# Performance work log

Hardware: AMD Instinct MI355X
Metric: run time of the kernel (lower is better)

The kernel has to match this reference:

```python
import jax, jax.numpy as jnp
import numpy as np

# module hyperparameters (from init_kwargs)
K = 32          # out_channels / features per branch
THRESH = 20.0   # firing threshold
KWTA = 4        # winners per branch
RF = 512        # rf_size (number of branches)
L = 2048        # receptive-field length
T = 32          # timesteps (leading 'batch' dim in SpykeTorch)
C = 1           # in_channels


def setup_inputs() -> dict:
    key = jax.random.key(0)
    k1, k2, k3 = jax.random.split(key, 3)
    rec_field = jax.random.uniform(k1, (T, C, RF, L), dtype=jnp.float32)
    W = jax.random.normal(k2, (RF, K, C, L), dtype=jnp.float32)  # per-branch local-conv weights
    reward = jax.random.normal(k3, (1, 1, RF), dtype=jnp.float32)
    return {"rec_field": rec_field, "W": W, "reward": reward}


def _winner_mask(thr, spikes):
    """SpykeTorch sf.get_k_winners for a single branch with 1x1 spatial output.
    thr, spikes: (T, K) thresholded potentials and their sign (0/1).
    Returns a (K,) 0/1 mask over the kwta winning features.
    Score = earliest-spike-dominant total potential, exactly as in SpykeTorch:
      first  = T - sum_t spikes           (first spike time, clamped)
      values = thr[first, k]
      total  = sum_t (spikes*values + spikes * max(spikes*values)*T)
    With 1x1 spatial, inhibition_radius has no effect; picking then zeroing a
    feature == distinct top-k over features with a nonzero check.
    """
    first = jnp.clip((T - spikes.sum(0)).astype(jnp.int32), 0, T - 1)          # (K,)
    vals_at_first = jnp.take_along_axis(thr, first[None, :], axis=0)[0]        # (K,)
    trunc = spikes * vals_at_first[None, :]                                    # (T, K)
    v = trunc.max() * T
    total = (trunc + spikes * v).sum(0)                                        # (K,)
    top_vals, top_idx = jax.lax.top_k(total, KWTA)
    valid = (top_vals != 0).astype(thr.dtype)
    return jnp.zeros((K,), thr.dtype).at[top_idx].max(valid)


def reference(rec_field, W, reward):
    # per-branch local convolution: kernel covers the whole (1,L) input -> 1x1 output
    pot = jnp.einsum('tcrl,rkcl->rtk', rec_field, W)        # (RF, T, K)
    # sf.fire: keep potentials strictly above threshold (F.threshold semantics)
    thr = jnp.where(pot > THRESH, pot, jnp.zeros((), pot.dtype))
    spikes = jnp.sign(thr)
    # kWTA winner masks per branch (coefs), then masked sign
    mask = jax.vmap(_winner_mask)(thr, spikes)              # (RF, K)
    out = jnp.sign(thr * mask[:, None, :])                  # (RF, T, K)
    # torch: cat(dim=2) -> (T,K,RF,1) -> squeeze -> (T,K,RF) -> unsqueeze(1) -> (T,1,K,RF)
    return jnp.transpose(out, (1, 2, 0))[:, None, :, :]
```

## Files before the change

kernel.cpp:

```cpp
#include <hip/hip_runtime.h>
#include <cstdint>


#define RFN 512
#define TN  32
#define KN  32
#define LN  2048
#define CHUNK 128
#define NITER (LN / CHUNK)

__global__ __launch_bounds__(256, 2) void column1_kernel(
    const float* __restrict__ rec,
    const float* __restrict__ wgt,
    float* __restrict__ out)
{
    __shared__ __align__(16) float lds[2 * 64 * CHUNK];
    const int r    = blockIdx.x;
    const int tid  = threadIdx.x;
    const int lane = tid & 63;
    const int wv   = tid >> 6;
    const int tg   = lane >> 3;
    const int kg   = lane & 7;

    const int c4 = tid & 31;
    const int r0 = tid >> 5;
    const float* gsrc[8];
    int ldoff[8];
#pragma unroll
    for (int s = 0; s < 8; ++s) {
        const int row = r0 + 8 * s;
        const float* g;
        if (row < 32) g = rec + ((size_t)(row * RFN + r)) * LN + (c4 << 2);
        else          g = wgt + ((size_t)(r * KN + (row - 32))) * LN + (c4 << 2);
        gsrc[s]  = g;
        ldoff[s] = row * CHUNK + ((c4 ^ (row & 7)) << 2);
    }

    float4 stage[8];
#pragma unroll
    for (int s = 0; s < 8; ++s) stage[s] = *(const float4*)gsrc[s];

    float acc[4][4];
#pragma unroll
    for (int jt = 0; jt < 4; ++jt)
#pragma unroll
        for (int jk = 0; jk < 4; ++jk) acc[jt][jk] = 0.0f;

    int p = 0;
    for (int it = 0; it < NITER; ++it) {
        float* buf = lds + p * (64 * CHUNK);
#pragma unroll
        for (int s = 0; s < 8; ++s) *(float4*)(buf + ldoff[s]) = stage[s];
        __syncthreads();
        if (it + 1 < NITER) {
#pragma unroll
            for (int s = 0; s < 8; ++s) {
                gsrc[s] += CHUNK;
                stage[s] = *(const float4*)gsrc[s];
            }
        }
        const float* rs = buf;
        const float* ws = buf + 32 * CHUNK;
#pragma unroll
        for (int q = 0; q < 8; ++q) {
            const int qg = (wv << 3) + q;
            float4 a[4], b[4];
#pragma unroll
            for (int j = 0; j < 4; ++j)
                a[j] = *(const float4*)(rs + (tg + 8 * j) * CHUNK + ((qg ^ tg) << 2));
#pragma unroll
            for (int j = 0; j < 4; ++j)
                b[j] = *(const float4*)(ws + (kg + 8 * j) * CHUNK + ((qg ^ kg) << 2));
#pragma unroll
            for (int jt = 0; jt < 4; ++jt)
#pragma unroll
                for (int jk = 0; jk < 4; ++jk) {
                    float v0 = fmaf(a[jt].x, b[jk].x, acc[jt][jk]);
                    v0 = fmaf(a[jt].y, b[jk].y, v0);
                    v0 = fmaf(a[jt].z, b[jk].z, v0);
                    acc[jt][jk] = fmaf(a[jt].w, b[jk].w, v0);
                }
        }
        p ^= 1;
    }

    float* red = lds;
#pragma unroll
    for (int jt = 0; jt < 4; ++jt)
#pragma unroll
        for (int jk = 0; jk < 4; ++jk)
            red[(wv << 10) + (tg + 8 * jt) * 32 + (kg + 8 * jk)] = acc[jt][jk];
    __syncthreads();

    float* thr_s = lds + 4096;
#pragma unroll
    for (int e = 0; e < 4; ++e) {
        const int o = (tid << 2) + e;
        float pv = red[o] + red[1024 + o] + red[2048 + o] + red[3072 + o];
        float th = (pv > 20.0f) ? pv : 0.0f;
        thr_s[(o >> 5) * 33 + (o & 31)] = th;
    }
    __syncthreads();

    float* nspk_s = lds + 4096 + 1056;
    float* vals_s = nspk_s + 32;
    float* cand_s = vals_s + 32;
    float* tot_s  = cand_s + 32;
    float* mask_s = tot_s + 32;

    if (tid < 32) {
        const int k = tid;
        int ns = 0;
        for (int t = 0; t < 32; ++t) ns += (thr_s[t * 33 + k] > 0.0f) ? 1 : 0;
        int first = 32 - ns; if (first > 31) first = 31;
        const float vf = thr_s[first * 33 + k];
        nspk_s[k] = (float)ns;
        vals_s[k] = vf;
        cand_s[k] = (ns > 0) ? vf : 0.0f;
        mask_s[k] = 0.0f;
    }
    __syncthreads();

    if (tid == 0) {
        float vm = 0.0f;
        for (int k = 0; k < 32; ++k) vm = fmaxf(vm, cand_s[k]);
        const float v = vm * 32.0f;
        for (int k = 0; k < 32; ++k) tot_s[k] = nspk_s[k] * (vals_s[k] + v);
        for (int sel = 0; sel < 4; ++sel) {
            int best = 0; float bv = -1.0f;
            for (int k = 0; k < 32; ++k) {
                const float tv = tot_s[k];
                if (tv > bv) { bv = tv; best = k; }
            }
            if (bv > 0.0f) mask_s[best] = 1.0f;
            tot_s[best] = -1.0f;
        }
    }
    __syncthreads();

#pragma unroll
    for (int e = 0; e < 4; ++e) {
        const int o = (tid << 2) + e;
        const int t = o >> 5, k = o & 31;
        out[(size_t)t * (KN * RFN) + k * RFN + r] =
            (thr_s[t * 33 + k] > 0.0f && mask_s[k] > 0.0f) ? 1.0f : 0.0f;
    }
}

extern "C" void kernel_launch(void* const* d_in, const int* in_sizes, int n_in,
                              void* d_out, int out_size, void* d_ws, size_t ws_size,
                              hipStream_t stream) {
    const float* rec = (const float*)d_in[0];
    const float* wgt = (const float*)d_in[1];
    float* out = (float*)d_out;
    column1_kernel<<<dim3(RFN), dim3(256), 0, stream>>>(rec, wgt, out);
}
```

Measured before the change: 324.1 us.

## Split reduction dimension across four blocks and add separate epilogue kernel

Each branch's 2048-length dot product is split into four segments handled by separate blocks, giving 2048 blocks instead of 512. Partial 32x32 results go to a workspace buffer, and a second kernel sums them and runs the threshold and k-winner selection. The chunk size is halved and the swizzle widened, which lowers shared memory per block and allows a higher occupancy hint. The aim is to fill the GPU's compute units and hide memory latency better on this bandwidth-bound load, at the cost of a second launch and a small workspace round trip.

After: 330.0 us. Within noise of the previous version (+1.8%).

```diff
diff --git a/kernel.cpp b/kernel.cpp
--- a/kernel.cpp
+++ b/kernel.cpp
@@ -6,39 +6,44 @@
 #define TN  32
 #define KN  32
 #define LN  2048
-#define CHUNK 128
-#define NITER (LN / CHUNK)
+#define SPLIT 4
+#define LSEG (LN / SPLIT)
+#define CHUNK 64
+#define NITER (LSEG / CHUNK)
 
-__global__ __launch_bounds__(256, 2) void column1_kernel(
+__global__ __launch_bounds__(256, 5) void column1_gemm(
     const float* __restrict__ rec,
     const float* __restrict__ wgt,
-    float* __restrict__ out)
+    float* __restrict__ wsout)
 {
     __shared__ __align__(16) float lds[2 * 64 * CHUNK];
-    const int r    = blockIdx.x;
+    const int bs   = blockIdx.x;
+    const int r    = bs >> 2;
+    const int sseg = bs & 3;
+    const int l0   = sseg * LSEG;
     const int tid  = threadIdx.x;
     const int lane = tid & 63;
     const int wv   = tid >> 6;
     const int tg   = lane >> 3;
     const int kg   = lane & 7;
 
-    const int c4 = tid & 31;
-    const int r0 = tid >> 5;
-    const float* gsrc[8];
-    int ldoff[8];
+    const int c4 = tid & 15;
+    const int r0 = tid >> 4;
+    const float* gsrc[4];
+    int ldoff[4];
 #pragma unroll
-    for (int s = 0; s < 8; ++s) {
-        const int row = r0 + 8 * s;
+    for (int s = 0; s < 4; ++s) {
+        const int row = r0 + 16 * s;
         const float* g;
-        if (row < 32) g = rec + ((size_t)(row * RFN + r)) * LN + (c4 << 2);
-        else          g = wgt + ((size_t)(r * KN + (row - 32))) * LN + (c4 << 2);
+        if (row < 32) g = rec + ((size_t)(row * RFN + r)) * LN + l0 + (c4 << 2);
+        else          g = wgt + ((size_t)(r * KN + (row - 32))) * LN + l0 + (c4 << 2);
         gsrc[s]  = g;
-        ldoff[s] = row * CHUNK + ((c4 ^ (row & 7)) << 2);
+        ldoff[s] = row * CHUNK + ((c4 ^ (row & 15)) << 2);
     }
 
-    float4 stage[8];
+    float4 stage[4];
 #pragma unroll
-    for (int s = 0; s < 8; ++s) stage[s] = *(const float4*)gsrc[s];
+    for (int s = 0; s < 4; ++s) stage[s] = *(const float4*)gsrc[s];
 
     float acc[4][4];
 #pragma unroll
@@ -50,27 +55,31 @@
     for (int it = 0; it < NITER; ++it) {
         float* buf = lds + p * (64 * CHUNK);
 #pragma unroll
-        for (int s = 0; s < 8; ++s) *(float4*)(buf + ldoff[s]) = stage[s];
+        for (int s = 0; s < 4; ++s) *(float4*)(buf + ldoff[s]) = stage[s];
         __syncthreads();
         if (it + 1 < NITER) {
 #pragma unroll
-            for (int s = 0; s < 8; ++s) {
+            for (int s = 0; s < 4; ++s) {
                 gsrc[s] += CHUNK;
                 stage[s] = *(const float4*)gsrc[s];
             }
         }
         const float* rs = buf;
-        const float* ws = buf + 32 * CHUNK;
+        const float* wsh = buf + 32 * CHUNK;
 #pragma unroll
-        for (int q = 0; q < 8; ++q) {
-            const int qg = (wv << 3) + q;
+        for (int q = 0; q < 4; ++q) {
+            const int qg = (wv << 2) + q;
             float4 a[4], b[4];
 #pragma unroll
-            for (int j = 0; j < 4; ++j)
-                a[j] = *(const float4*)(rs + (tg + 8 * j) * CHUNK + ((qg ^ tg) << 2));
+            for (int j = 0; j < 4; ++j) {
+                const int row = tg + 8 * j;
+                a[j] = *(const float4*)(rs + row * CHUNK + ((qg ^ (row & 15)) << 2));
+            }
 #pragma unroll
-            for (int j = 0; j < 4; ++j)
-                b[j] = *(const float4*)(ws + (kg + 8 * j) * CHUNK + ((qg ^ kg) << 2));
+            for (int j = 0; j < 4; ++j) {
+                const int row = kg + 8 * j;
+                b[j] = *(const float4*)(wsh + row * CHUNK + ((qg ^ (row & 15)) << 2));
+            }
 #pragma unroll
             for (int jt = 0; jt < 4; ++jt)
 #pragma unroll
@@ -92,21 +101,45 @@
             red[(wv << 10) + (tg + 8 * jt) * 32 + (kg + 8 * jk)] = acc[jt][jk];
     __syncthreads();
 
-    float* thr_s = lds + 4096;
+    const int o = tid << 2;
+    float4 p0 = *(const float4*)(red + o);
+    float4 p1 = *(const float4*)(red + 1024 + o);
+    float4 p2 = *(const float4*)(red + 2048 + o);
+    float4 p3 = *(const float4*)(red + 3072 + o);
+    float4 pv;
+    pv.x = p0.x + p1.x + p2.x + p3.x;
+    pv.y = p0.y + p1.y + p2.y + p3.y;
+    pv.z = p0.z + p1.z + p2.z + p3.z;
+    pv.w = p0.w + p1.w + p2.w + p3.w;
+    *(float4*)(wsout + (size_t)(r * SPLIT + sseg) * 1024 + o) = pv;
+}
+
+__global__ __launch_bounds__(256) void column1_epilogue(
+    const float* __restrict__ wsin,
+    float* __restrict__ out)
+{
+    __shared__ float thr_s[32 * 33];
+    __shared__ float nspk_s[32], vals_s[32], cand_s[32], tot_s[32], mask_s[32];
+    const int r   = blockIdx.x;
+    const int tid = threadIdx.x;
+    const float* base = wsin + (size_t)r * (SPLIT * 1024);
+
+    const int o = tid << 2;
+    float4 p0 = *(const float4*)(base + o);
+    float4 p1 = *(const float4*)(base + 1024 + o);
+    float4 p2 = *(const float4*)(base + 2048 + o);
+    float4 p3 = *(const float4*)(base + 3072 + o);
+    float pv[4] = { p0.x + p1.x + p2.x + p3.x,
+                    p0.y + p1.y + p2.y + p3.y,
+                    p0.z + p1.z + p2.z + p3.z,
+                    p0.w + p1.w + p2.w + p3.w };
 #pragma unroll
     for (int e = 0; e < 4; ++e) {
-        const int o = (tid << 2) + e;
-        float pv = red[o] + red[1024 + o] + red[2048 + o] + red[3072 + o];
-        float th = (pv > 20.0f) ? pv : 0.0f;
-        thr_s[(o >> 5) * 33 + (o & 31)] = th;
+        const int oo = o + e;
+        const float th = (pv[e] > 20.0f) ? pv[e] : 0.0f;
+        thr_s[(oo >> 5) * 33 + (oo & 31)] = th;
     }
     __syncthreads();
-
-    float* nspk_s = lds + 4096 + 1056;
-    float* vals_s = nspk_s + 32;
-    float* cand_s = vals_s + 32;
-    float* tot_s  = cand_s + 32;
-    float* mask_s = tot_s + 32;
 
     if (tid < 32) {
         const int k = tid;
@@ -140,8 +173,8 @@
 
 #pragma unroll
     for (int e = 0; e < 4; ++e) {
-        const int o = (tid << 2) + e;
-        const int t = o >> 5, k = o & 31;
+        const int oo = o + e;
+        const int t = oo >> 5, k = oo & 31;
         out[(size_t)t * (KN * RFN) + k * RFN + r] =
             (thr_s[t * 33 + k] > 0.0f && mask_s[k] > 0.0f) ? 1.0f : 0.0f;
     }
@@ -153,5 +186,7 @@
     const float* rec = (const float*)d_in[0];
     const float* wgt = (const float*)d_in[1];
     float* out = (float*)d_out;
-    column1_kernel<<<dim3(RFN), dim3(256), 0, stream>>>(rec, wgt, out);
+    float* ws  = (float*)d_ws;
+    column1_gemm<<<dim3(RFN * SPLIT), dim3(256), 0, stream>>>(rec, wgt, ws);
+    column1_epilogue<<<dim3(RFN), dim3(256), 0, stream>>>(ws, out);
 }
```

## Double chunk size, per-wave contiguous row loads with nontemporal hints

Applied to the files above, without the earlier changes.

Doubles the L-chunk staged per iteration to 256, which halves the number of barrier-separated iterations and doubles LDS use to 128 KB. Each wave now loads 16 full rows of 1 KB with lane-contiguous addresses instead of the previous scattered mapping. The XOR swizzle widens to 16, and launch bounds drop to one block per CU. Global loads and output stores use nontemporal hints, since the streamed data is never reused. The risks are lower occupancy for hiding latency and higher register pressure from 16 staged float4 values per thread.

After: 300.6 us. 7.2% less time.

```diff
diff --git a/kernel.cpp b/kernel.cpp
--- a/kernel.cpp
+++ b/kernel.cpp
@@ -1,15 +1,17 @@
 #include <hip/hip_runtime.h>
 #include <cstdint>
 
+
+typedef float vf4 __attribute__((ext_vector_type(4)));
 
 #define RFN 512
 #define TN  32
 #define KN  32
 #define LN  2048
-#define CHUNK 128
+#define CHUNK 256
 #define NITER (LN / CHUNK)
 
-__global__ __launch_bounds__(256, 2) void column1_kernel(
+__global__ __launch_bounds__(256, 1) void column1_kernel(
     const float* __restrict__ rec,
     const float* __restrict__ wgt,
     float* __restrict__ out)
@@ -22,23 +24,24 @@
     const int tg   = lane >> 3;
     const int kg   = lane & 7;
 
-    const int c4 = tid & 31;
-    const int r0 = tid >> 5;
-    const float* gsrc[8];
-    int ldoff[8];
+    const int row0 = wv << 4;
+    const float* gbase;
+    size_t rstride;
+    if (wv < 2) { gbase = rec + ((size_t)(row0 * RFN + r)) * LN;        rstride = (size_t)RFN * LN; }
+    else        { gbase = wgt + ((size_t)(r * KN + (row0 - 32))) * LN;  rstride = LN; }
+    gbase += (lane << 2);
+
+    int ldoff[16];
 #pragma unroll
-    for (int s = 0; s < 8; ++s) {
-        const int row = r0 + 8 * s;
-        const float* g;
-        if (row < 32) g = rec + ((size_t)(row * RFN + r)) * LN + (c4 << 2);
-        else          g = wgt + ((size_t)(r * KN + (row - 32))) * LN + (c4 << 2);
-        gsrc[s]  = g;
-        ldoff[s] = row * CHUNK + ((c4 ^ (row & 7)) << 2);
+    for (int s = 0; s < 16; ++s) {
+        const int row = row0 + s;
+        ldoff[s] = row * CHUNK + ((lane ^ (row & 15)) << 2);
     }
 
-    float4 stage[8];
+    vf4 stage[16];
 #pragma unroll
-    for (int s = 0; s < 8; ++s) stage[s] = *(const float4*)gsrc[s];
+    for (int s = 0; s < 16; ++s)
+        stage[s] = __builtin_nontemporal_load((const vf4*)(gbase + s * rstride));
 
     float acc[4][4];
 #pragma unroll
@@ -46,31 +49,32 @@
 #pragma unroll
         for (int jk = 0; jk < 4; ++jk) acc[jt][jk] = 0.0f;
 
-    int p = 0;
     for (int it = 0; it < NITER; ++it) {
-        float* buf = lds + p * (64 * CHUNK);
+        float* buf = lds + (it & 1) * (64 * CHUNK);
 #pragma unroll
-        for (int s = 0; s < 8; ++s) *(float4*)(buf + ldoff[s]) = stage[s];
+        for (int s = 0; s < 16; ++s) *(vf4*)(buf + ldoff[s]) = stage[s];
         __syncthreads();
         if (it + 1 < NITER) {
+            const float* g = gbase + (size_t)(it + 1) * CHUNK;
 #pragma unroll
-            for (int s = 0; s < 8; ++s) {
-                gsrc[s] += CHUNK;
-                stage[s] = *(const float4*)gsrc[s];
+            for (int s = 0; s < 16; ++s)
+                stage[s] = __builtin_nontemporal_load((const vf4*)(g + s * rstride));
+        }
+        const float* rs  = buf;
+#pragma unroll
+        for (int q = 0; q < 16; ++q) {
+            const int qg = (wv << 4) + q;
+            vf4 a[4], b[4];
+#pragma unroll
+            for (int j = 0; j < 4; ++j) {
+                const int row = tg + 8 * j;
+                a[j] = *(const vf4*)(rs + row * CHUNK + ((qg ^ (row & 15)) << 2));
             }
-        }
-        const float* rs = buf;
-        const float* ws = buf + 32 * CHUNK;
 #pragma unroll
-        for (int q = 0; q < 8; ++q) {
-            const int qg = (wv << 3) + q;
-            float4 a[4], b[4];
-#pragma unroll
-            for (int j = 0; j < 4; ++j)
-                a[j] = *(const float4*)(rs + (tg + 8 * j) * CHUNK + ((qg ^ tg) << 2));
-#pragma unroll
-            for (int j = 0; j < 4; ++j)
-                b[j] = *(const float4*)(ws + (kg + 8 * j) * CHUNK + ((qg ^ kg) << 2));
+            for (int j = 0; j < 4; ++j) {
+                const int row = 32 + kg + 8 * j;
+                b[j] = *(const vf4*)(rs + row * CHUNK + ((qg ^ (row & 15)) << 2));
+            }
 #pragma unroll
             for (int jt = 0; jt < 4; ++jt)
 #pragma unroll
@@ -81,7 +85,6 @@
                     acc[jt][jk] = fmaf(a[jt].w, b[jk].w, v0);
                 }
         }
-        p ^= 1;
     }
 
     float* red = lds;
@@ -142,8 +145,8 @@
     for (int e = 0; e < 4; ++e) {
         const int o = (tid << 2) + e;
         const int t = o >> 5, k = o & 31;
-        out[(size_t)t * (KN * RFN) + k * RFN + r] =
-            (thr_s[t * 33 + k] > 0.0f && mask_s[k] > 0.0f) ? 1.0f : 0.0f;
+        const float v = (thr_s[t * 33 + k] > 0.0f && mask_s[k] > 0.0f) ? 1.0f : 0.0f;
+        __builtin_nontemporal_store(v, out + (size_t)t * (KN * RFN) + k * RFN + r);
     }
 }
 
```
